# Kernel tuning notes

Hardware: AMD Instinct MI355X
Metric: run time of the kernel (lower is better)

Reference implementation:

```python
import jax, jax.numpy as jnp
import numpy as np

H, U_DIM = 64, 64
N = H * U_DIM
COEF_GAMMA = 0.4


def setup_inputs() -> dict:
    key = jax.random.key(0)
    ks = jax.random.split(key, 7)
    inp = jax.random.normal(ks[0], (H, U_DIM), jnp.float32)
    L = jax.random.normal(ks[1], (H, U_DIM), jnp.float32)
    th_P = 0.1 * jax.random.normal(ks[2], (H, U_DIM), jnp.float32)
    entries_mask = jax.random.uniform(ks[3], (H, U_DIM)) < 0.5  # observed-entry mask
    # D_tilda: dense (HU, HU) regularizer operator (e.g. a discrete-difference Gram);
    # symmetrized and small so the full operator stays well-conditioned.
    G = jax.random.normal(ks[4], (N, N), jnp.float32) / np.sqrt(N)
    D_tilda = 0.05 * (G + G.T)
    S = jax.random.normal(ks[5], (H, H), jnp.float32) / np.sqrt(H)
    return {
        "inp": inp,
        "L": L,
        "entries_mask": entries_mask,
        "D_tilda": D_tilda,
        "th_P": th_P,
        "v": jnp.float32(0.1),
        "neta": jnp.float32(0.5),
        "lamda1": jnp.float32(0.1),
        "lamda2": jnp.float32(0.1),
        "rho": jnp.float32(1.0),
        "S": S,
    }


def _svtC(x, tau):
    # torch.svd: x = Um diag(s) V^T ; here Vh = V^T (square 64x64 case).
    Um, s, Vh = jnp.linalg.svd(x, full_matrices=False)
    s_thr = jax.nn.relu(s - tau * s[0])  # threshold relative to top singular value
    return (Um * s_thr) @ Vh


def reference(inp, L, entries_mask, D_tilda, th_P, v, neta, lamda1, lamda2, rho, S):
    tau = jax.nn.sigmoid(v) * COEF_GAMMA
    q = entries_mask.reshape(N).astype(jnp.float32)          # diag of Q_tilda
    StS = S.T @ S                                            # (H, H)
    S_tilda = jnp.kron(jnp.eye(U_DIM, dtype=jnp.float32), StS)  # (HU, HU)
    vec = rho * (L - th_P) + jnp.where(entries_mask, inp, jnp.float32(0.0))
    A = (jnp.diag(q) + lamda1 * D_tilda + lamda2 * S_tilda
         + rho * jnp.eye(N, dtype=jnp.float32))
    x = jnp.linalg.solve(A, vec.reshape(N)).reshape(H, U_DIM)  # == inv(A) @ vec
    Ltmp = _svtC(x + th_P, tau)
    Ptmp = th_P + neta * (x - Ltmp)
    return Ltmp, Ptmp
```

## Files before the change

kernel.cpp:

```cpp
#include <hip/hip_runtime.h>
#include <hip/hip_bf16.h>

#define NN 4096
#define NITER 4
#define NSWEEP 5
#define MCS 68

#define OFF_STS  64
#define OFF_QRHO (OFF_STS + NN)
#define OFF_DINV (OFF_QRHO + NN)
#define OFF_Y0   (OFF_DINV + NN)
#define OFF_Y1   (OFF_Y0 + NN)
#define OFF_X0   (OFF_Y1 + NN)
#define OFF_X1   (OFF_X0 + NN)
#define OFF_R0   (OFF_X1 + NN)
#define OFF_R1   (OFF_R0 + NN)
#define OFF_P0   (OFF_R1 + NN)
#define OFF_P1   (OFF_P0 + NN)
#define DH_OFF_BYTES 196608
#define WS_NEED_BF16 (DH_OFF_BYTES + (size_t)NN * NN * 2)

typedef unsigned int uint;
__device__ inline float lo2f(uint w){ return __uint_as_float(w << 16); }
__device__ inline float hi2f(uint w){ return __uint_as_float(w & 0xffff0000u); }
__device__ inline uint f2b(float f){
    uint u = __float_as_uint(f);
    return (u + 0x7FFFu + ((u >> 16) & 1u)) >> 16;
}
__device__ inline float rsum16(float x){
    int a = __builtin_amdgcn_update_dpp(0, __float_as_int(x), 0xB1, 0xF, 0xF, true);
    float s = x + __int_as_float(a);
    int b = __builtin_amdgcn_update_dpp(0, __float_as_int(s), 0x4E, 0xF, 0xF, true);
    s = s + __int_as_float(b);
    int c = __builtin_amdgcn_update_dpp(0, __float_as_int(s), 0x141, 0xF, 0xF, true);
    s = s + __int_as_float(c);
    int d = __builtin_amdgcn_update_dpp(0, __float_as_int(s), 0x140, 0xF, 0xF, true);
    s = s + __int_as_float(d);
    return s;
}

__global__ void k_prep(const float* __restrict__ inp, const float* __restrict__ L,
                       const int*  __restrict__ mask, const float* __restrict__ thP,
                       const float* __restrict__ S,
                       const float* __restrict__ l2p, const float* __restrict__ rhop,
                       float* __restrict__ wf){
    int t = blockIdx.x * 256 + threadIdx.x;
    if(blockIdx.x == 0 && threadIdx.x < 64) wf[threadIdx.x] = 0.f;
    int r = t >> 6, c = t & 63;
    float acc = 0.f, acc2 = 0.f;
    for(int h = 0; h < 64; ++h){
        float sr = S[h*64 + r];
        float sc = S[h*64 + c];
        acc  += sr * sc;
        acc2 += sc * sc;
    }
    wf[OFF_STS + t] = acc;
    float rho = rhop[0], l2 = l2p[0];
    float q = (mask[t] != 0) ? 1.f : 0.f;
    float bi = rho * (L[t] - thP[t]) + q * inp[t];
    float dinv = 1.f / (q + rho + l2 * acc2);
    wf[OFF_QRHO + t] = q + rho;
    wf[OFF_DINV + t] = dinv;
    wf[OFF_X0 + t]   = 0.f;
    wf[OFF_R0 + t]   = bi;
    wf[OFF_P0 + t]   = bi * dinv;
}

__device__ inline void cg_prologue(float* __restrict__ wf,
                                   const float* __restrict__ rold, const float* __restrict__ pold,
                                   const float* __restrict__ xold, const float* __restrict__ yold,
                                   float* __restrict__ rnew, float* __restrict__ pnew,
                                   float* __restrict__ xnew,
                                   int slot_old, float* __restrict__ psh,
                                   float* __restrict__ red){
    int tid = threadIdx.x;
    const float* dinv = wf + OFF_DINV;
    float4 r4[4], d4[4];
    float part = 0.f;
    #pragma unroll
    for(int k = 0; k < 4; ++k){
        r4[k] = ((const float4*)rold)[tid + k*256];
        d4[k] = ((const float4*)dinv)[tid + k*256];
        part += r4[k].x*r4[k].x*d4[k].x + r4[k].y*r4[k].y*d4[k].y
              + r4[k].z*r4[k].z*d4[k].z + r4[k].w*r4[k].w*d4[k].w;
    }
    for(int m = 32; m >= 1; m >>= 1) part += __shfl_xor(part, m, 64);
    int wave = tid >> 6, lane = tid & 63;
    if(lane == 0) red[wave] = part;
    __syncthreads();
    float rzold = red[0] + red[1] + red[2] + red[3];
    float alpha = rzold / wf[slot_old];
    float4 rn[4], zn[4];
    float part2 = 0.f;
    #pragma unroll
    for(int k = 0; k < 4; ++k){
        float4 y4 = ((const float4*)yold)[tid + k*256];
        rn[k].x = r4[k].x - alpha*y4.x;  rn[k].y = r4[k].y - alpha*y4.y;
        rn[k].z = r4[k].z - alpha*y4.z;  rn[k].w = r4[k].w - alpha*y4.w;
        zn[k].x = rn[k].x*d4[k].x;  zn[k].y = rn[k].y*d4[k].y;
        zn[k].z = rn[k].z*d4[k].z;  zn[k].w = rn[k].w*d4[k].w;
        part2 += rn[k].x*zn[k].x + rn[k].y*zn[k].y + rn[k].z*zn[k].z + rn[k].w*zn[k].w;
    }
    for(int m = 32; m >= 1; m >>= 1) part2 += __shfl_xor(part2, m, 64);
    __syncthreads();
    if(lane == 0) red[wave] = part2;
    __syncthreads();
    float rznew = red[0] + red[1] + red[2] + red[3];
    float beta = rznew / rzold;
    bool b0 = (blockIdx.x == 0);
    #pragma unroll
    for(int k = 0; k < 4; ++k){
        float4 po = ((const float4*)pold)[tid + k*256];
        float4 pn;
        pn.x = zn[k].x + beta*po.x;  pn.y = zn[k].y + beta*po.y;
        pn.z = zn[k].z + beta*po.z;  pn.w = zn[k].w + beta*po.w;
        ((float4*)psh)[tid + k*256] = pn;
        if(b0){
            ((float4*)pnew)[tid + k*256] = pn;
            ((float4*)rnew)[tid + k*256] = rn[k];
            float4 xo = ((const float4*)xold)[tid + k*256];
            float4 xn;
            xn.x = xo.x + alpha*po.x;  xn.y = xo.y + alpha*po.y;
            xn.z = xo.z + alpha*po.z;  xn.w = xo.w + alpha*po.w;
            ((float4*)xnew)[tid + k*256] = xn;
        }
    }
    __syncthreads();
}

__launch_bounds__(256)
__global__ void k_step_h(const unsigned short* __restrict__ Dh,
                         const float* __restrict__ l1p, const float* __restrict__ l2p,
                         float* __restrict__ wf,
                         const float* __restrict__ rold, const float* __restrict__ pold,
                         const float* __restrict__ xold, const float* __restrict__ yold,
                         float* __restrict__ rnew, float* __restrict__ pnew,
                         float* __restrict__ xnew, float* __restrict__ ynew,
                         int slot_old, int slot_new){
    __shared__ float psh[NN];
    __shared__ float red[4];
    int tid = threadIdx.x;
    cg_prologue(wf, rold, pold, xold, yold, rnew, pnew, xnew, slot_old, psh, red);

    float l1 = l1p[0], l2 = l2p[0];
    int wave = tid >> 6, lane = tid & 63;
    int row = blockIdx.x * 4 + wave;
    int h = row >> 6, u = row & 63;
    const float* qrho = wf + OFF_QRHO;
    const float* StS  = wf + OFF_STS;

    const unsigned short* Drow = Dh + (size_t)row * NN;
    float dacc = 0.f;
    for(int j = 0; j < 8; ++j){
        int c0 = j*512 + lane*8;
        uint4 dv = *(const uint4*)(Drow + c0);
        float4 pa = *(const float4*)(psh + c0);
        float4 pb = *(const float4*)(psh + c0 + 4);
        dacc += lo2f(dv.x)*pa.x + hi2f(dv.x)*pa.y
              + lo2f(dv.y)*pa.z + hi2f(dv.y)*pa.w
              + lo2f(dv.z)*pb.x + hi2f(dv.z)*pb.y
              + lo2f(dv.w)*pb.z + hi2f(dv.w)*pb.w;
    }
    float sacc = StS[u*64 + lane] * psh[h*64 + lane];
    float val = l1 * dacc + l2 * sacc;
    for(int m = 32; m >= 1; m >>= 1) val += __shfl_xor(val, m, 64);
    if(lane == 0){
        float yi = val + qrho[row] * psh[row];
        ynew[row] = yi;
        red[wave] = yi * psh[row];
    }
    __syncthreads();
    if(tid == 0) atomicAdd(&wf[slot_new], red[0] + red[1] + red[2] + red[3]);
}

__launch_bounds__(256)
__global__ void k_step_fc(const float* __restrict__ D, unsigned short* __restrict__ Dh,
                          const float* __restrict__ l1p, const float* __restrict__ l2p,
                          float* __restrict__ wf, const float* __restrict__ p0,
                          float* __restrict__ ynew, int slot_new){
    __shared__ float psh[NN];
    __shared__ float red[4];
    int tid = threadIdx.x;
    for(int k = 0; k < 4; ++k)
        ((float4*)psh)[tid + k*256] = ((const float4*)p0)[tid + k*256];
    __syncthreads();

    float l1 = l1p[0], l2 = l2p[0];
    int wave = tid >> 6, lane = tid & 63;
    int row = blockIdx.x * 4 + wave;
    int h = row >> 6, u = row & 63;
    const float* qrho = wf + OFF_QRHO;
    const float* StS  = wf + OFF_STS;

    const float* Drow = D + (size_t)row * NN;
    unsigned short* Dhrow = Dh + (size_t)row * NN;
    float dacc = 0.f;
    for(int j = 0; j < 16; ++j){
        int c0 = j*256 + lane*4;
        float4 dv = *(const float4*)(Drow + c0);
        float4 pa = *(const float4*)(psh + c0);
        dacc += dv.x*pa.x + dv.y*pa.y + dv.z*pa.z + dv.w*pa.w;
        uint2 o;
        o.x = f2b(dv.x) | (f2b(dv.y) << 16);
        o.y = f2b(dv.z) | (f2b(dv.w) << 16);
        *(uint2*)(Dhrow + c0) = o;
    }
    float sacc = StS[u*64 + lane] * psh[h*64 + lane];
    float val = l1 * dacc + l2 * sacc;
    for(int m = 32; m >= 1; m >>= 1) val += __shfl_xor(val, m, 64);
    if(lane == 0){
        float yi = val + qrho[row] * psh[row];
        ynew[row] = yi;
        red[wave] = yi * psh[row];
    }
    __syncthreads();
    if(tid == 0) atomicAdd(&wf[slot_new], red[0] + red[1] + red[2] + red[3]);
}

__launch_bounds__(256)
__global__ void k_step_f(const float* __restrict__ D,
                         const float* __restrict__ l1p, const float* __restrict__ l2p,
                         float* __restrict__ wf,
                         const float* __restrict__ rold, const float* __restrict__ pold,
                         const float* __restrict__ xold, const float* __restrict__ yold,
                         float* __restrict__ rnew, float* __restrict__ pnew,
                         float* __restrict__ xnew, float* __restrict__ ynew,
                         int slot_old, int slot_new, int do_pro){
    __shared__ float psh[NN];
    __shared__ float red[4];
    int tid = threadIdx.x;
    if(do_pro){
        cg_prologue(wf, rold, pold, xold, yold, rnew, pnew, xnew, slot_old, psh, red);
    } else {
        for(int k = 0; k < 4; ++k)
            ((float4*)psh)[tid + k*256] = ((const float4*)pold)[tid + k*256];
        __syncthreads();
    }
    float l1 = l1p[0], l2 = l2p[0];
    int wave = tid >> 6, lane = tid & 63;
    int row = blockIdx.x * 4 + wave;
    int h = row >> 6, u = row & 63;
    const float* qrho = wf + OFF_QRHO;
    const float* StS  = wf + OFF_STS;
    const float* Drow = D + (size_t)row * NN;
    float dacc = 0.f;
    for(int j = 0; j < 16; ++j){
        int c0 = j*256 + lane*4;
        float4 dv = *(const float4*)(Drow + c0);
        float4 pa = *(const float4*)(psh + c0);
        dacc += dv.x*pa.x + dv.y*pa.y + dv.z*pa.z + dv.w*pa.w;
    }
    float sacc = StS[u*64 + lane] * psh[h*64 + lane];
    float val = l1 * dacc + l2 * sacc;
    for(int m = 32; m >= 1; m >>= 1) val += __shfl_xor(val, m, 64);
    if(lane == 0){
        float yi = val + qrho[row] * psh[row];
        ynew[row] = yi;
        red[wave] = yi * psh[row];
    }
    __syncthreads();
    if(tid == 0) atomicAdd(&wf[slot_new], red[0] + red[1] + red[2] + red[3]);
}

#define P_MA(par) (POOL + (par)*2176)
#define P_MB(par) (POOL + 4352 + (par)*2176)
#define P_XSH     (POOL + 8704)
#define P_TSH     (POOL)
#define P_WC      (POOL + 4352)
#define DOT4(u,v) ((u).x*(v).x + (u).y*(v).y + (u).z*(v).z + (u).w*(v).w)

__launch_bounds__(512)
__global__ void k_svt(const float* __restrict__ thP, const float* __restrict__ vp,
                      const float* __restrict__ netap,
                      float* __restrict__ wf,
                      const float* __restrict__ rlast, const float* __restrict__ plast,
                      const float* __restrict__ xlast, int slot_last,
                      float* __restrict__ out){
    __shared__ float POOL[12800];
    __shared__ float s2[64], coef3[64];
    __shared__ float smax_sh;
    __shared__ float redv[8];
    int tid = threadIdx.x;
    float* Xsh = P_XSH;

    {
        const float* dinv = wf + OFF_DINV;
        float part = 0.f;
        #pragma unroll
        for(int k = 0; k < 2; ++k){
            float4 r4 = ((const float4*)rlast)[tid + k*512];
            float4 d4 = ((const float4*)dinv)[tid + k*512];
            part += r4.x*r4.x*d4.x + r4.y*r4.y*d4.y + r4.z*r4.z*d4.z + r4.w*r4.w*d4.w;
        }
        for(int m = 32; m >= 1; m >>= 1) part += __shfl_xor(part, m, 64);
        if((tid & 63) == 0) redv[tid >> 6] = part;
        __syncthreads();
        float rz = redv[0] + redv[1] + redv[2] + redv[3]
                 + redv[4] + redv[5] + redv[6] + redv[7];
        float a = rz / wf[slot_last];
        #pragma unroll
        for(int k = 0; k < 2; ++k){
            float4 x4 = ((const float4*)xlast)[tid + k*512];
            float4 p4 = ((const float4*)plast)[tid + k*512];
            float4 t4 = ((const float4*)thP)[tid + k*512];
            float4 v;
            v.x = x4.x + a*p4.x + t4.x;  v.y = x4.y + a*p4.y + t4.y;
            v.z = x4.z + a*p4.z + t4.z;  v.w = x4.w + a*p4.w + t4.w;
            ((float4*)Xsh)[tid + k*512] = v;
        }
    }
    __syncthreads();

    int g  = tid >> 4;
    int sl = tid & 15;
    float4 A, B;
    {
        int ca = 2*g, cb = 2*g + 1, r0 = sl*4;
        A.x = Xsh[(r0+0)*64+ca]; A.y = Xsh[(r0+1)*64+ca];
        A.z = Xsh[(r0+2)*64+ca]; A.w = Xsh[(r0+3)*64+ca];
        B.x = Xsh[(r0+0)*64+cb]; B.y = Xsh[(r0+1)*64+cb];
        B.z = Xsh[(r0+2)*64+cb]; B.w = Xsh[(r0+3)*64+cb];
    }
    float aa = rsum16(DOT4(A,A));
    float bb = rsum16(DOT4(B,B));

    const int total = NSWEEP * 63;
    for(int gr = 0; gr < total; ++gr){
        float cc = rsum16(DOT4(A,B));
        float cs = 1.f, sn = 0.f, t = 0.f;
        if(fabsf(cc) > 1e-30f){
            float zeta = (bb - aa) * 0.5f * __builtin_amdgcn_rcpf(cc);
            t = copysignf(__builtin_amdgcn_rcpf(fabsf(zeta) +
                          __builtin_amdgcn_sqrtf(1.f + zeta*zeta)), zeta);
            cs = __builtin_amdgcn_rsqf(1.f + t*t);
            sn = t * cs;
        }
        float naN = aa - t*cc;
        float nbN = bb + t*cc;
        if(gr != total - 1){
            int par = gr & 1;
            float* MAp = P_MA(par);
            float* MBp = P_MB(par);
            float4 nb;
            nb.x = sn*A.x + cs*B.x; nb.y = sn*A.y + cs*B.y;
            nb.z = sn*A.z + cs*B.z; nb.w = sn*A.w + cs*B.w;
            float* cbB = (g == 0) ? (MAp + 1*MCS) : (MBp + (g-1)*MCS);
            *(float4*)(cbB + sl*4) = nb;
            if(sl == 0) cbB[64] = nbN;
            float4 na;
            na.x = cs*A.x - sn*B.x; na.y = cs*A.y - sn*B.y;
            na.z = cs*A.z - sn*B.z; na.w = cs*A.w - sn*B.w;
            if(g >= 1 && g <= 30){
                float* cbA = MAp + (g+1)*MCS;
                *(float4*)(cbA + sl*4) = na;
                if(sl == 0) cbA[64] = naN;
            }
            __syncthreads();
            float4 nA = na;  float nAa = naN;
            float4 nB = na;  float nBb = naN;
            if(g >= 1){
                const float* ra = MAp + g*MCS;
                nA = *(const float4*)(ra + sl*4);
                nAa = ra[64];
            }
            if(g <= 30){
                const float* rb = MBp + g*MCS;
                nB = *(const float4*)(rb + sl*4);
                nBb = rb[64];
            }
            A = nA; B = nB; aa = nAa; bb = nBb;
        } else {
            float4 na;
            na.x = cs*A.x - sn*B.x; na.y = cs*A.y - sn*B.y;
            na.z = cs*A.z - sn*B.z; na.w = cs*A.w - sn*B.w;
            float4 nbf;
            nbf.x = sn*A.x + cs*B.x; nbf.y = sn*A.y + cs*B.y;
            nbf.z = sn*A.z + cs*B.z; nbf.w = sn*A.w + cs*B.w;
            A = na; B = nbf;
        }
    }
    {
        float fa = rsum16(DOT4(A,A));
        float fb = rsum16(DOT4(B,B));
        __syncthreads();
        float* Wc = P_WC;
        *(float4*)(Wc + (2*g)*MCS + sl*4)   = A;
        *(float4*)(Wc + (2*g+1)*MCS + sl*4) = B;
        if(sl == 0){ s2[2*g] = fa; s2[2*g+1] = fb; }
    }
    __syncthreads();
    if(tid == 0){
        float sm = 0.f;
        for(int c = 0; c < 64; ++c) sm = fmaxf(sm, s2[c]);
        smax_sh = sqrtf(sm);
    }
    __syncthreads();
    if(tid < 64){
        float s = sqrtf(s2[tid]);
        float v = vp[0];
        float tau = 0.4f / (1.f + expf(-v));
        float thr = tau * smax_sh;
        coef3[tid] = (s > thr && s > 1e-20f) ? (s - thr) / (s*s*s) : 0.f;
    }
    __syncthreads();

    const float* Wc = P_WC;
    float* Tsh = P_TSH;
    {
        int kk = tid >> 3;
        int j0 = (tid & 7) * 8;
        float acc[8];
        #pragma unroll
        for(int j = 0; j < 8; ++j) acc[j] = 0.f;
        for(int r = 0; r < 64; ++r){
            float wk = Wc[kk*MCS + r];
            const float* xr = Xsh + r*64 + j0;
            float4 x0 = *(const float4*)(xr);
            float4 x1 = *(const float4*)(xr + 4);
            acc[0]+=wk*x0.x; acc[1]+=wk*x0.y; acc[2]+=wk*x0.z; acc[3]+=wk*x0.w;
            acc[4]+=wk*x1.x; acc[5]+=wk*x1.y; acc[6]+=wk*x1.z; acc[7]+=wk*x1.w;
        }
        float c3 = coef3[kk];
        float* tr = Tsh + kk*64 + j0;
        float4 t0, t1;
        t0.x = c3*acc[0]; t0.y = c3*acc[1]; t0.z = c3*acc[2]; t0.w = c3*acc[3];
        t1.x = c3*acc[4]; t1.y = c3*acc[5]; t1.z = c3*acc[6]; t1.w = c3*acc[7];
        *(float4*)(tr)     = t0;
        *(float4*)(tr + 4) = t1;
    }
    __syncthreads();

    {
        float neta = netap[0];
        int i  = tid >> 3;
        int j0 = (tid & 7) * 8;
        float acc[8];
        #pragma unroll
        for(int j = 0; j < 8; ++j) acc[j] = 0.f;
        for(int kk = 0; kk < 64; ++kk){
            float wik = Wc[kk*MCS + i];
            const float* tr = Tsh + kk*64 + j0;
            float4 t0 = *(const float4*)(tr);
            float4 t1 = *(const float4*)(tr + 4);
            acc[0]+=wik*t0.x; acc[1]+=wik*t0.y; acc[2]+=wik*t0.z; acc[3]+=wik*t0.w;
            acc[4]+=wik*t1.x; acc[5]+=wik*t1.y; acc[6]+=wik*t1.z; acc[7]+=wik*t1.w;
        }
        int n0 = i*64 + j0;
        #pragma unroll
        for(int c = 0; c < 2; ++c){
            float4 th = *(const float4*)(thP + n0 + 4*c);
            float4 lt, pt;
            lt.x = acc[4*c+0]; lt.y = acc[4*c+1]; lt.z = acc[4*c+2]; lt.w = acc[4*c+3];
            float4 xs = *(const float4*)(Xsh + n0 + 4*c);
            pt.x = th.x + neta * (xs.x - th.x - lt.x);
            pt.y = th.y + neta * (xs.y - th.y - lt.y);
            pt.z = th.z + neta * (xs.z - th.z - lt.z);
            pt.w = th.w + neta * (xs.w - th.w - lt.w);
            *(float4*)(out + n0 + 4*c)      = lt;
            *(float4*)(out + NN + n0 + 4*c) = pt;
        }
    }
}

extern "C" void kernel_launch(void* const* d_in, const int* in_sizes, int n_in,
                              void* d_out, int out_size, void* d_ws, size_t ws_size,
                              hipStream_t stream){
    const float* inp  = (const float*)d_in[0];
    const float* L    = (const float*)d_in[1];
    const int*   mask = (const int*)  d_in[2];
    const float* D    = (const float*)d_in[3];
    const float* thP  = (const float*)d_in[4];
    const float* vS   = (const float*)d_in[5];
    const float* neta = (const float*)d_in[6];
    const float* l1   = (const float*)d_in[7];
    const float* l2   = (const float*)d_in[8];
    const float* rho  = (const float*)d_in[9];
    const float* S    = (const float*)d_in[10];
    float* wf = (float*)d_ws;
    float* out = (float*)d_out;
    const bool use_bf16 = (ws_size >= WS_NEED_BF16);
    unsigned short* Dh = (unsigned short*)((char*)d_ws + DH_OFF_BYTES);

    float* Xb[2] = { wf + OFF_X0, wf + OFF_X1 };
    float* Rb[2] = { wf + OFF_R0, wf + OFF_R1 };
    float* Pb[2] = { wf + OFF_P0, wf + OFF_P1 };
    float* Yb[2] = { wf + OFF_Y0, wf + OFF_Y1 };

    k_prep<<<16, 256, 0, stream>>>(inp, L, mask, thP, S, l2, rho, wf);
    if(use_bf16){
        k_step_fc<<<1024, 256, 0, stream>>>(D, Dh, l1, l2, wf, Pb[0], Yb[0], 8);
        for(int j = 1; j < NITER; ++j){
            int ro = (j+1)&1, wr = j&1;
            k_step_h<<<1024, 256, 0, stream>>>(Dh, l1, l2, wf,
                Rb[ro], Pb[ro], Xb[ro], Yb[ro],
                Rb[wr], Pb[wr], Xb[wr], Yb[wr], 8+j-1, 8+j);
        }
    } else {
        k_step_f<<<1024, 256, 0, stream>>>(D, l1, l2, wf,
            Rb[0], Pb[0], Xb[0], Yb[0], Rb[1], Pb[1], Xb[1], Yb[0], 8, 8, 0);
        for(int j = 1; j < NITER; ++j){
            int ro = (j+1)&1, wr = j&1;
            k_step_f<<<1024, 256, 0, stream>>>(D, l1, l2, wf,
                Rb[ro], Pb[ro], Xb[ro], Yb[ro],
                Rb[wr], Pb[wr], Xb[wr], Yb[wr], 8+j-1, 8+j, 1);
        }
    }
    const int lp = (NITER-1)&1;
    k_svt<<<1, 512, 0, stream>>>(thP, vS, neta, wf, Rb[lp], Pb[lp], Xb[lp], 8+NITER-1, out);
}
```

Measured before the change: 326.8 us.

## Fuse prep into first CG step and replace atomics with per-block partial sums

Removes the separate k_prep launch in the bf16 path: every block of the first step kernel now recomputes the preconditioned initial direction and the StS/diag terms itself, and 16 blocks write the canonical workspace arrays. The atomicAdd accumulation of p^T y into a zeroed slot is replaced by per-block partial sums in a ping-pong buffer, which each later kernel reduces in its prologue. This saves one launch and the atomic traffic and zero-init, at the cost of redundant per-block recomputation of S column norms and the initial vector, plus a 1024-element reduction per block.

```diff
diff --git a/kernel.cpp b/kernel.cpp
--- a/kernel.cpp
+++ b/kernel.cpp
@@ -17,6 +17,8 @@
 #define OFF_R1   (OFF_R0 + NN)
 #define OFF_P0   (OFF_R1 + NN)
 #define OFF_P1   (OFF_P0 + NN)
+#define OFF_PTY0 (OFF_P1 + NN)
+#define OFF_PTY1 (OFF_PTY0 + 1024)
 #define DH_OFF_BYTES 196608
 #define WS_NEED_BF16 (DH_OFF_BYTES + (size_t)NN * NN * 2)
 
@@ -45,7 +47,6 @@
                        const float* __restrict__ l2p, const float* __restrict__ rhop,
                        float* __restrict__ wf){
     int t = blockIdx.x * 256 + threadIdx.x;
-    if(blockIdx.x == 0 && threadIdx.x < 64) wf[threadIdx.x] = 0.f;
     int r = t >> 6, c = t & 63;
     float acc = 0.f, acc2 = 0.f;
     for(int h = 0; h < 64; ++h){
@@ -71,7 +72,8 @@
                                    const float* __restrict__ xold, const float* __restrict__ yold,
                                    float* __restrict__ rnew, float* __restrict__ pnew,
                                    float* __restrict__ xnew,
-                                   int slot_old, float* __restrict__ psh,
+                                   const float* __restrict__ pty_read,
+                                   float* __restrict__ psh,
                                    float* __restrict__ red){
     int tid = threadIdx.x;
     const float* dinv = wf + OFF_DINV;
@@ -84,12 +86,17 @@
         part += r4[k].x*r4[k].x*d4[k].x + r4[k].y*r4[k].y*d4[k].y
               + r4[k].z*r4[k].z*d4[k].z + r4[k].w*r4[k].w*d4[k].w;
     }
-    for(int m = 32; m >= 1; m >>= 1) part += __shfl_xor(part, m, 64);
+    float pp = pty_read[tid] + pty_read[tid+256] + pty_read[tid+512] + pty_read[tid+768];
+    for(int m = 32; m >= 1; m >>= 1){
+        part += __shfl_xor(part, m, 64);
+        pp   += __shfl_xor(pp, m, 64);
+    }
     int wave = tid >> 6, lane = tid & 63;
-    if(lane == 0) red[wave] = part;
+    if(lane == 0){ red[wave] = part; red[4+wave] = pp; }
     __syncthreads();
     float rzold = red[0] + red[1] + red[2] + red[3];
-    float alpha = rzold / wf[slot_old];
+    float ptys  = red[4] + red[5] + red[6] + red[7];
+    float alpha = rzold / ptys;
     float4 rn[4], zn[4];
     float part2 = 0.f;
     #pragma unroll
@@ -129,68 +136,54 @@
 }
 
 __launch_bounds__(256)
-__global__ void k_step_h(const unsigned short* __restrict__ Dh,
-                         const float* __restrict__ l1p, const float* __restrict__ l2p,
-                         float* __restrict__ wf,
-                         const float* __restrict__ rold, const float* __restrict__ pold,
-                         const float* __restrict__ xold, const float* __restrict__ yold,
-                         float* __restrict__ rnew, float* __restrict__ pnew,
-                         float* __restrict__ xnew, float* __restrict__ ynew,
-                         int slot_old, int slot_new){
+__global__ void k_fc(const float* __restrict__ D, unsigned short* __restrict__ Dh,
+                     const float* __restrict__ inp, const float* __restrict__ L,
+                     const int*  __restrict__ mask, const float* __restrict__ thP,
+                     const float* __restrict__ S,
+                     const float* __restrict__ l1p, const float* __restrict__ l2p,
+                     const float* __restrict__ rhop,
+                     float* __restrict__ wf, float* __restrict__ pty_out){
     __shared__ float psh[NN];
-    __shared__ float red[4];
+    __shared__ float red[8];
+    __shared__ float cparts[256];
     int tid = threadIdx.x;
-    cg_prologue(wf, rold, pold, xold, yold, rnew, pnew, xnew, slot_old, psh, red);
-
-    float l1 = l1p[0], l2 = l2p[0];
     int wave = tid >> 6, lane = tid & 63;
     int row = blockIdx.x * 4 + wave;
-    int h = row >> 6, u = row & 63;
-    const float* qrho = wf + OFF_QRHO;
-    const float* StS  = wf + OFF_STS;
-
-    const unsigned short* Drow = Dh + (size_t)row * NN;
-    float dacc = 0.f;
-    for(int j = 0; j < 8; ++j){
-        int c0 = j*512 + lane*8;
-        uint4 dv = *(const uint4*)(Drow + c0);
-        float4 pa = *(const float4*)(psh + c0);
-        float4 pb = *(const float4*)(psh + c0 + 4);
-        dacc += lo2f(dv.x)*pa.x + hi2f(dv.x)*pa.y
-              + lo2f(dv.y)*pa.z + hi2f(dv.y)*pa.w
-              + lo2f(dv.z)*pb.x + hi2f(dv.z)*pb.y
-              + lo2f(dv.w)*pb.z + hi2f(dv.w)*pb.w;
-    }
-    float sacc = StS[u*64 + lane] * psh[h*64 + lane];
-    float val = l1 * dacc + l2 * sacc;
-    for(int m = 32; m >= 1; m >>= 1) val += __shfl_xor(val, m, 64);
-    if(lane == 0){
-        float yi = val + qrho[row] * psh[row];
-        ynew[row] = yi;
-        red[wave] = yi * psh[row];
-    }
-    __syncthreads();
-    if(tid == 0) atomicAdd(&wf[slot_new], red[0] + red[1] + red[2] + red[3]);
-}
-
-__launch_bounds__(256)
-__global__ void k_step_fc(const float* __restrict__ D, unsigned short* __restrict__ Dh,
-                          const float* __restrict__ l1p, const float* __restrict__ l2p,
-                          float* __restrict__ wf, const float* __restrict__ p0,
-                          float* __restrict__ ynew, int slot_new){
-    __shared__ float psh[NN];
-    __shared__ float red[4];
-    int tid = threadIdx.x;
-    for(int k = 0; k < 4; ++k)
-        ((float4*)psh)[tid + k*256] = ((const float4*)p0)[tid + k*256];
-    __syncthreads();
-
-    float l1 = l1p[0], l2 = l2p[0];
-    int wave = tid >> 6, lane = tid & 63;
-    int row = blockIdx.x * 4 + wave;
-    int h = row >> 6, u = row & 63;
-    const float* qrho = wf + OFF_QRHO;
-    const float* StS  = wf + OFF_STS;
+    int u = row & 63, h = row >> 6;
+    float l1 = l1p[0], l2 = l2p[0], rho = rhop[0];
+
+    {
+        float cp = 0.f;
+        for(int hh = wave*16; hh < wave*16 + 16; ++hh){
+            float sv = S[hh*64 + lane];
+            cp += sv * sv;
+        }
+        cparts[wave*64 + lane] = cp;
+    }
+    float stv = 0.f;
+    for(int hh = 0; hh < 64; ++hh)
+        stv += S[hh*64 + u] * S[hh*64 + lane];
+    if(row < 64) wf[OFF_STS + row*64 + lane] = stv;
+    __syncthreads();
+
+    int c = tid & 63;
+    float cs4 = cparts[c] + cparts[64+c] + cparts[128+c] + cparts[192+c];
+    bool canon = (blockIdx.x < 16);
+    for(int k = 0; k < 16; ++k){
+        int t = tid + k*256;
+        float q = (mask[t] != 0) ? 1.f : 0.f;
+        float bi = rho * (L[t] - thP[t]) + q * inp[t];
+        float dinv = 1.f / (q + rho + l2 * cs4);
+        psh[t] = bi * dinv;
+        if(canon && k == (int)blockIdx.x){
+            wf[OFF_QRHO + t] = q + rho;
+            wf[OFF_DINV + t] = dinv;
+            wf[OFF_X0 + t]   = 0.f;
+            wf[OFF_R0 + t]   = bi;
+            wf[OFF_P0 + t]   = bi * dinv;
+        }
+    }
+    __syncthreads();
 
     const float* Drow = D + (size_t)row * NN;
     unsigned short* Dhrow = Dh + (size_t)row * NN;
@@ -205,6 +198,52 @@
         o.y = f2b(dv.z) | (f2b(dv.w) << 16);
         *(uint2*)(Dhrow + c0) = o;
     }
+    float sacc = stv * psh[h*64 + lane];
+    float val = l1 * dacc + l2 * sacc;
+    for(int m = 32; m >= 1; m >>= 1) val += __shfl_xor(val, m, 64);
+    if(lane == 0){
+        float qr = ((mask[row] != 0) ? 1.f : 0.f) + rho;
+        float yi = val + qr * psh[row];
+        (wf + OFF_Y0)[row] = yi;
+        red[wave] = yi * psh[row];
+    }
+    __syncthreads();
+    if(tid == 0) pty_out[blockIdx.x] = red[0] + red[1] + red[2] + red[3];
+}
+
+__launch_bounds__(256)
+__global__ void k_step_h(const unsigned short* __restrict__ Dh,
+                         const float* __restrict__ l1p, const float* __restrict__ l2p,
+                         float* __restrict__ wf,
+                         const float* __restrict__ rold, const float* __restrict__ pold,
+                         const float* __restrict__ xold, const float* __restrict__ yold,
+                         float* __restrict__ rnew, float* __restrict__ pnew,
+                         float* __restrict__ xnew, float* __restrict__ ynew,
+                         const float* __restrict__ pty_read, float* __restrict__ pty_write){
+    __shared__ float psh[NN];
+    __shared__ float red[8];
+    int tid = threadIdx.x;
+    cg_prologue(wf, rold, pold, xold, yold, rnew, pnew, xnew, pty_read, psh, red);
+
+    float l1 = l1p[0], l2 = l2p[0];
+    int wave = tid >> 6, lane = tid & 63;
+    int row = blockIdx.x * 4 + wave;
+    int h = row >> 6, u = row & 63;
+    const float* qrho = wf + OFF_QRHO;
+    const float* StS  = wf + OFF_STS;
+
+    const unsigned short* Drow = Dh + (size_t)row * NN;
+    float dacc = 0.f;
+    for(int j = 0; j < 8; ++j){
+        int c0 = j*512 + lane*8;
+        uint4 dv = *(const uint4*)(Drow + c0);
+        float4 pa = *(const float4*)(psh + c0);
+        float4 pb = *(const float4*)(psh + c0 + 4);
+        dacc += lo2f(dv.x)*pa.x + hi2f(dv.x)*pa.y
+              + lo2f(dv.y)*pa.z + hi2f(dv.y)*pa.w
+              + lo2f(dv.z)*pb.x + hi2f(dv.z)*pb.y
+              + lo2f(dv.w)*pb.z + hi2f(dv.w)*pb.w;
+    }
     float sacc = StS[u*64 + lane] * psh[h*64 + lane];
     float val = l1 * dacc + l2 * sacc;
     for(int m = 32; m >= 1; m >>= 1) val += __shfl_xor(val, m, 64);
@@ -214,7 +253,7 @@
         red[wave] = yi * psh[row];
     }
     __syncthreads();
-    if(tid == 0) atomicAdd(&wf[slot_new], red[0] + red[1] + red[2] + red[3]);
+    if(tid == 0) pty_write[blockIdx.x] = red[0] + red[1] + red[2] + red[3];
 }
 
 __launch_bounds__(256)
@@ -225,12 +264,13 @@
                          const float* __restrict__ xold, const float* __restrict__ yold,
                          float* __restrict__ rnew, float* __restrict__ pnew,
                          float* __restrict__ xnew, float* __restrict__ ynew,
-                         int slot_old, int slot_new, int do_pro){
+                         const float* __restrict__ pty_read, float* __restrict__ pty_write,
+                         int do_pro){
     __shared__ float psh[NN];
-    __shared__ float red[4];
+    __shared__ float red[8];
     int tid = threadIdx.x;
     if(do_pro){
-        cg_prologue(wf, rold, pold, xold, yold, rnew, pnew, xnew, slot_old, psh, red);
+        cg_prologue(wf, rold, pold, xold, yold, rnew, pnew, xnew, pty_read, psh, red);
     } else {
         for(int k = 0; k < 4; ++k)
             ((float4*)psh)[tid + k*256] = ((const float4*)pold)[tid + k*256];
@@ -259,7 +299,7 @@
         red[wave] = yi * psh[row];
     }
     __syncthreads();
-    if(tid == 0) atomicAdd(&wf[slot_new], red[0] + red[1] + red[2] + red[3]);
+    if(tid == 0) pty_write[blockIdx.x] = red[0] + red[1] + red[2] + red[3];
 }
 
 #define P_MA(par) (POOL + (par)*2176)
@@ -274,12 +314,13 @@
                       const float* __restrict__ netap,
                       float* __restrict__ wf,
                       const float* __restrict__ rlast, const float* __restrict__ plast,
-                      const float* __restrict__ xlast, int slot_last,
+                      const float* __restrict__ xlast,
+                      const float* __restrict__ ptyp,
                       float* __restrict__ out){
     __shared__ float POOL[12800];
     __shared__ float s2[64], coef3[64];
     __shared__ float smax_sh;
-    __shared__ float redv[8];
+    __shared__ float redv[16];
     int tid = threadIdx.x;
     float* Xsh = P_XSH;
 
@@ -292,12 +333,18 @@
             float4 d4 = ((const float4*)dinv)[tid + k*512];
             part += r4.x*r4.x*d4.x + r4.y*r4.y*d4.y + r4.z*r4.z*d4.z + r4.w*r4.w*d4.w;
         }
-        for(int m = 32; m >= 1; m >>= 1) part += __shfl_xor(part, m, 64);
-        if((tid & 63) == 0) redv[tid >> 6] = part;
+        float pp = ptyp[tid] + ptyp[tid + 512];
+        for(int m = 32; m >= 1; m >>= 1){
+            part += __shfl_xor(part, m, 64);
+            pp   += __shfl_xor(pp, m, 64);
+        }
+        if((tid & 63) == 0){ redv[tid >> 6] = part; redv[8 + (tid >> 6)] = pp; }
         __syncthreads();
         float rz = redv[0] + redv[1] + redv[2] + redv[3]
                  + redv[4] + redv[5] + redv[6] + redv[7];
-        float a = rz / wf[slot_last];
+        float ptys = redv[8] + redv[9] + redv[10] + redv[11]
+                   + redv[12] + redv[13] + redv[14] + redv[15];
+        float a = rz / ptys;
         #pragma unroll
         for(int k = 0; k < 2; ++k){
             float4 x4 = ((const float4*)xlast)[tid + k*512];
@@ -481,30 +528,36 @@
     const bool use_bf16 = (ws_size >= WS_NEED_BF16);
     unsigned short* Dh = (unsigned short*)((char*)d_ws + DH_OFF_BYTES);
 
-    float* Xb[2] = { wf + OFF_X0, wf + OFF_X1 };
-    float* Rb[2] = { wf + OFF_R0, wf + OFF_R1 };
-    float* Pb[2] = { wf + OFF_P0, wf + OFF_P1 };
-    float* Yb[2] = { wf + OFF_Y0, wf + OFF_Y1 };
-
-    k_prep<<<16, 256, 0, stream>>>(inp, L, mask, thP, S, l2, rho, wf);
+    float* Xb[2]  = { wf + OFF_X0, wf + OFF_X1 };
+    float* Rb[2]  = { wf + OFF_R0, wf + OFF_R1 };
+    float* Pb[2]  = { wf + OFF_P0, wf + OFF_P1 };
+    float* Yb[2]  = { wf + OFF_Y0, wf + OFF_Y1 };
+    float* pty[2] = { wf + OFF_PTY0, wf + OFF_PTY1 };
+
     if(use_bf16){
-        k_step_fc<<<1024, 256, 0, stream>>>(D, Dh, l1, l2, wf, Pb[0], Yb[0], 8);
+        k_fc<<<1024, 256, 0, stream>>>(D, Dh, inp, L, mask, thP, S,
+                                       l1, l2, rho, wf, pty[0]);
         for(int j = 1; j < NITER; ++j){
             int ro = (j+1)&1, wr = j&1;
             k_step_h<<<1024, 256, 0, stream>>>(Dh, l1, l2, wf,
                 Rb[ro], Pb[ro], Xb[ro], Yb[ro],
-                Rb[wr], Pb[wr], Xb[wr], Yb[wr], 8+j-1, 8+j);
+                Rb[wr], Pb[wr], Xb[wr], Yb[wr],
+                pty[(j-1)&1], pty[j&1]);
         }
     } else {
+        k_prep<<<16, 256, 0, stream>>>(inp, L, mask, thP, S, l2, rho, wf);
         k_step_f<<<1024, 256, 0, stream>>>(D, l1, l2, wf,
-            Rb[0], Pb[0], Xb[0], Yb[0], Rb[1], Pb[1], Xb[1], Yb[0], 8, 8, 0);
+            Rb[0], Pb[0], Xb[0], Yb[0], Rb[1], Pb[1], Xb[1], Yb[0],
+            pty[0], pty[0], 0);
         for(int j = 1; j < NITER; ++j){
             int ro = (j+1)&1, wr = j&1;
             k_step_f<<<1024, 256, 0, stream>>>(D, l1, l2, wf,
                 Rb[ro], Pb[ro], Xb[ro], Yb[ro],
-                Rb[wr], Pb[wr], Xb[wr], Yb[wr], 8+j-1, 8+j, 1);
+                Rb[wr], Pb[wr], Xb[wr], Yb[wr],
+                pty[(j-1)&1], pty[j&1], 1);
         }
     }
     const int lp = (NITER-1)&1;
-    k_svt<<<1, 512, 0, stream>>>(thP, vS, neta, wf, Rb[lp], Pb[lp], Xb[lp], 8+NITER-1, out);
-}
+    k_svt<<<1, 512, 0, stream>>>(thP, vS, neta, wf, Rb[lp], Pb[lp], Xb[lp],
+                                 pty[lp], out);
+}
```

New measurement: 292.9 us. 1.12x faster.
